# Performance work log

Measured on AMD Instinct MI355X. Metric: run time of the kernel, lower is better.

## Reference

```python
import jax, jax.numpy as jnp
import numpy as np

B, T, U = 64, 512, 1024
TIME_STEP = 0.008

# Rieke cone phototransduction parameters (scaleFac = 1, values are final)
PR = dict(sigma=22.0, phi=22.0, eta=2000.0, beta=9.0, cgmp2cur=0.01,
          cgmphill=3.0, cdark=1.0, betaSlow=0.4, hillcoef=4.0,
          hillaffinity=0.5, gamma=10.0, gdark=20.0)


def setup_inputs() -> dict:
    key = jax.random.key(0)
    X = jax.random.uniform(key, (B, T, U), dtype=jnp.float32)  # light intensity >= 0
    inp = {"X_fun": X}
    for name, v in PR.items():
        inp[name] = jnp.full((1, U), v, dtype=jnp.float32)  # flax param shape (1, units)
    return inp


def reference(X_fun, sigma, phi, eta, beta, cgmp2cur, cgmphill, cdark,
              betaSlow, hillcoef, hillaffinity, gamma, gdark):
    # Derived constants (as in runRiekeModel preamble)
    darkCurrent = gdark ** cgmphill * cgmp2cur / 2
    gdark_e = (2 * darkCurrent / cgmp2cur) ** (1 / cgmphill)
    cur2ca = beta * cdark / darkCurrent
    smax = eta / phi * gdark_e * (1 + (cdark / hillaffinity) ** hillcoef)

    Bd, Td, Ud = X_fun.shape
    ones = jnp.ones((Bd, Ud), X_fun.dtype)
    g0 = gdark_e * ones
    s0 = gdark_e * eta / phi * ones
    c0 = cdark * ones
    cslow0 = cdark * ones
    r0 = X_fun[:, 0, :] * gamma / sigma
    p0 = (eta + r0) / phi

    def step(carry, x_prev):
        g, s, c, cslow, p, r = carry
        r_n = r + TIME_STEP * (-sigma * r) + gamma * x_prev
        p_n = p + TIME_STEP * (r + eta - phi * p)
        c_n = c + TIME_STEP * (cur2ca * cgmp2cur * g ** cgmphill
                               / (1 + cslow / cdark) - beta * c)
        cslow_n = cslow - TIME_STEP * (betaSlow * (cslow - c))
        s_n = smax / (1 + (c_n / hillaffinity) ** hillcoef)
        g_n = g + TIME_STEP * (s - p * g)
        return (g_n, s_n, c_n, cslow_n, p_n, r_n), g_n

    xs = jnp.moveaxis(X_fun[:, :-1, :], 1, 0)  # [T-1, B, U], step pnt uses X[:, pnt-1, :]
    _, g_seq = jax.lax.scan(step, (g0, s0, c0, cslow0, p0, r0), xs)
    # g[:, 0, :] stays zero in the original (loop starts at pnt=1)
    g = jnp.concatenate([jnp.zeros((Bd, 1, Ud), X_fun.dtype),
                         jnp.moveaxis(g_seq, 0, 1)], axis=1)
    return -(cgmp2cur * g ** cgmphill) / 2
```

## Files before the change

### kernel.cpp

```cpp
#include <hip/hip_runtime.h>
#include <math.h>


#define TT 512
#define UU 1024
#define UN 16
#define DTSTEP 0.008f

template <bool FAST>
__device__ __forceinline__ void run_chain(
    const float* __restrict__ xrow, float* __restrict__ orow,
    float sigma, float phi, float eta, float beta, float cgmp2cur,
    float cgmphill, float cdark, float betaSlow, float hillcoef,
    float hillaff, float gam, float gdark)
{
    const float darkCurrent = powf(gdark, cgmphill) * cgmp2cur * 0.5f;
    const float gdark_e = powf(2.0f * darkCurrent / cgmp2cur, 1.0f / cgmphill);
    const float cur2ca = beta * cdark / darkCurrent;
    const float smax = eta / phi * gdark_e *
                       (1.0f + powf(cdark / hillaff, hillcoef));

    const float Ar   = 1.0f - DTSTEP * sigma;
    const float icd  = 1.0f / cdark;
    const float kc   = cur2ca * cgmp2cur;
    const float iha  = 1.0f / hillaff;
    const float outk = -0.5f * cgmp2cur;
    const float dtbs = DTSTEP * betaSlow;

    float g  = gdark_e;
    float s  = gdark_e * eta / phi;
    float c  = cdark;
    float cs = cdark;
    float r, p;
    {
        float x0 = xrow[0];
        r = x0 * gam / sigma;
        p = (eta + r) / phi;
    }
    float gp = FAST ? g * g * g : __powf(g, cgmphill);

    orow[0] = 0.0f;

    auto step = [&](float x, float& outv) {
        float rn  = fmaf(Ar, r, gam * x);
        float pn  = fmaf(DTSTEP, (r + eta) - phi * p, p);
        float den = fmaf(cs, icd, 1.0f);
        float cn  = fmaf(DTSTEP,
                         fmaf(-beta, c, kc * gp * __builtin_amdgcn_rcpf(den)),
                         c);
        float csn = fmaf(-dtbs, cs - c, cs);
        float sn;
        if (FAST) {
            float t2 = cn * iha;
            t2 *= t2;
            sn = smax * __builtin_amdgcn_rcpf(fmaf(t2, t2, 1.0f));
        } else {
            sn = smax / (1.0f + __powf(cn * iha, hillcoef));
        }
        float gn  = fmaf(DTSTEP, fmaf(-p, g, s), g);
        float gpn = FAST ? gn * gn * gn : __powf(gn, cgmphill);
        outv = outk * gpn;
        g = gn; s = sn; c = cn; cs = csn; p = pn; r = rn; gp = gpn;
    };

    float bufA[UN], bufB[UN], ob[UN];

#pragma unroll
    for (int k = 0; k < UN; ++k) bufA[k] = xrow[k * UU];

    const float* xln = xrow + UN * UU;
    float* op = orow + UU;

    for (int pair = 0; pair < 15; ++pair) {
#pragma unroll
        for (int k = 0; k < UN; ++k) bufB[k] = xln[k * UU];
        __builtin_amdgcn_sched_barrier(0);
#pragma unroll
        for (int k = 0; k < UN; ++k) step(bufA[k], ob[k]);
        __builtin_amdgcn_sched_barrier(0);
#pragma unroll
        for (int k = 0; k < UN; ++k) op[k * UU] = ob[k];
        __builtin_amdgcn_sched_barrier(0);
        xln += UN * UU; op += UN * UU;

#pragma unroll
        for (int k = 0; k < UN; ++k) bufA[k] = xln[k * UU];
        __builtin_amdgcn_sched_barrier(0);
#pragma unroll
        for (int k = 0; k < UN; ++k) step(bufB[k], ob[k]);
        __builtin_amdgcn_sched_barrier(0);
#pragma unroll
        for (int k = 0; k < UN; ++k) op[k * UU] = ob[k];
        __builtin_amdgcn_sched_barrier(0);
        xln += UN * UU; op += UN * UU;
    }

#pragma unroll
    for (int k = 0; k < UN; ++k) bufB[k] = xln[k * UU];
    __builtin_amdgcn_sched_barrier(0);
#pragma unroll
    for (int k = 0; k < UN; ++k) step(bufA[k], ob[k]);
    __builtin_amdgcn_sched_barrier(0);
#pragma unroll
    for (int k = 0; k < UN; ++k) op[k * UU] = ob[k];
    op += UN * UU;

#pragma unroll
    for (int k = 0; k < UN - 1; ++k) {
        float o;
        step(bufB[k], o);
        op[k * UU] = o;
    }
}

__global__ __launch_bounds__(256, 1) void prfr_kernel(
    const float* __restrict__ X,
    const float* __restrict__ sigma_p, const float* __restrict__ phi_p,
    const float* __restrict__ eta_p,   const float* __restrict__ beta_p,
    const float* __restrict__ cgmp2cur_p, const float* __restrict__ cgmphill_p,
    const float* __restrict__ cdark_p, const float* __restrict__ betaSlow_p,
    const float* __restrict__ hillcoef_p, const float* __restrict__ hillaff_p,
    const float* __restrict__ gamma_p, const float* __restrict__ gdark_p,
    float* __restrict__ out, int total)
{
    const int idx = blockIdx.x * blockDim.x + threadIdx.x;
    if (idx >= total) return;
    const int u = idx & (UU - 1);
    const int b = idx >> 10;

    const float* xrow = X + (long)b * (TT * UU) + u;
    float* orow = out + (long)b * (TT * UU) + u;

    const float sigma = sigma_p[u], phi = phi_p[u], eta = eta_p[u];
    const float beta = beta_p[u], cgmp2cur = cgmp2cur_p[u];
    const float cgmphill = cgmphill_p[u], cdark = cdark_p[u];
    const float betaSlow = betaSlow_p[u], hillcoef = hillcoef_p[u];
    const float hillaff = hillaff_p[u], gam = gamma_p[u], gdark = gdark_p[u];

    if (cgmphill == 3.0f && hillcoef == 4.0f) {
        run_chain<true>(xrow, orow, sigma, phi, eta, beta, cgmp2cur, cgmphill,
                        cdark, betaSlow, hillcoef, hillaff, gam, gdark);
    } else {
        run_chain<false>(xrow, orow, sigma, phi, eta, beta, cgmp2cur, cgmphill,
                         cdark, betaSlow, hillcoef, hillaff, gam, gdark);
    }
}

extern "C" void kernel_launch(void* const* d_in, const int* in_sizes, int n_in,
                              void* d_out, int out_size, void* d_ws, size_t ws_size,
                              hipStream_t stream)
{
    const float* X = (const float*)d_in[0];
    const int B = in_sizes[0] / (TT * UU);
    const int total = B * UU;
    const int block = 256;
    const int grid = (total + block - 1) / block;
    prfr_kernel<<<grid, block, 0, stream>>>(
        X,
        (const float*)d_in[1],  (const float*)d_in[2],  (const float*)d_in[3],
        (const float*)d_in[4],  (const float*)d_in[5],  (const float*)d_in[6],
        (const float*)d_in[7],  (const float*)d_in[8],  (const float*)d_in[9],
        (const float*)d_in[10], (const float*)d_in[11], (const float*)d_in[12],
        (float*)d_out, total);
}
```

Baseline: 258.9 us.

## Prefetch input tiles into LDS via async global_load_lds double buffering

Replaces the register-based double-buffered input prefetch with asynchronous global-to-LDS loads (global_load_lds) into a per-wave double buffer in shared memory. Explicit s_waitcnt vmcnt counts gate reuse of the buffer. Output stores are now interleaved with the recurrence steps instead of being batched. The aim is to free registers and overlap input fetch with the serial recurrence, at the cost of extra LDS reads and reliance on hand-counted outstanding memory operations for correctness.

```diff
diff --git a/kernel.cpp b/kernel.cpp
--- a/kernel.cpp
+++ b/kernel.cpp
@@ -7,9 +7,17 @@
 #define UN 16
 #define DTSTEP 0.008f
 
+__device__ __forceinline__ void gload_lds(const float* g, float* l) {
+    __builtin_amdgcn_global_load_lds(
+        (__attribute__((address_space(1))) void*)(uintptr_t)g,
+        (__attribute__((address_space(3))) void*)l, 4, 0, 0);
+}
+
 template <bool FAST>
 __device__ __forceinline__ void run_chain(
     const float* __restrict__ xrow, float* __restrict__ orow,
+    float* __restrict__ swave,
+    int lane,
     float sigma, float phi, float eta, float beta, float cgmp2cur,
     float cgmphill, float cdark, float betaSlow, float hillcoef,
     float hillaff, float gam, float gdark)
@@ -63,53 +71,53 @@
         g = gn; s = sn; c = cn; cs = csn; p = pn; r = rn; gp = gpn;
     };
 
-    float bufA[UN], bufB[UN], ob[UN];
+#pragma unroll
+    for (int k = 0; k < UN; ++k)
+        gload_lds(xrow + k * UU, swave + k * 64);
 
-#pragma unroll
-    for (int k = 0; k < UN; ++k) bufA[k] = xrow[k * UU];
-
-    const float* xln = xrow + UN * UU;
+    const float* xst = xrow + UN * UU;
     float* op = orow + UU;
 
-    for (int pair = 0; pair < 15; ++pair) {
+    for (int n = 0; n < TT / UN - 1; ++n) {
+        if (n == 0) {
+            asm volatile("s_waitcnt vmcnt(0)" ::: "memory");
+        } else {
+            asm volatile("s_waitcnt vmcnt(16)" ::: "memory");
+        }
+        __builtin_amdgcn_sched_barrier(0);
+        const int p2 = (n & 1) * (UN * 64);
+        float xa[UN];
 #pragma unroll
-        for (int k = 0; k < UN; ++k) bufB[k] = xln[k * UU];
+        for (int k = 0; k < UN; ++k) xa[k] = swave[p2 + k * 64 + lane];
+        __builtin_amdgcn_sched_barrier(0);
+        const int q2 = ((n & 1) ^ 1) * (UN * 64);
+#pragma unroll
+        for (int k = 0; k < UN; ++k)
+            gload_lds(xst + k * UU, swave + q2 + k * 64);
         __builtin_amdgcn_sched_barrier(0);
 #pragma unroll
-        for (int k = 0; k < UN; ++k) step(bufA[k], ob[k]);
-        __builtin_amdgcn_sched_barrier(0);
-#pragma unroll
-        for (int k = 0; k < UN; ++k) op[k * UU] = ob[k];
-        __builtin_amdgcn_sched_barrier(0);
-        xln += UN * UU; op += UN * UU;
-
-#pragma unroll
-        for (int k = 0; k < UN; ++k) bufA[k] = xln[k * UU];
-        __builtin_amdgcn_sched_barrier(0);
-#pragma unroll
-        for (int k = 0; k < UN; ++k) step(bufB[k], ob[k]);
-        __builtin_amdgcn_sched_barrier(0);
-#pragma unroll
-        for (int k = 0; k < UN; ++k) op[k * UU] = ob[k];
-        __builtin_amdgcn_sched_barrier(0);
-        xln += UN * UU; op += UN * UU;
+        for (int k = 0; k < UN; ++k) {
+            float o;
+            step(xa[k], o);
+            op[k * UU] = o;
+        }
+        xst += UN * UU;
+        op += UN * UU;
     }
 
+    asm volatile("s_waitcnt vmcnt(16)" ::: "memory");
+    __builtin_amdgcn_sched_barrier(0);
+    {
+        const int p2 = (31 & 1) * (UN * 64);
+        float xa[UN];
 #pragma unroll
-    for (int k = 0; k < UN; ++k) bufB[k] = xln[k * UU];
-    __builtin_amdgcn_sched_barrier(0);
+        for (int k = 0; k < UN; ++k) xa[k] = swave[p2 + k * 64 + lane];
 #pragma unroll
-    for (int k = 0; k < UN; ++k) step(bufA[k], ob[k]);
-    __builtin_amdgcn_sched_barrier(0);
-#pragma unroll
-    for (int k = 0; k < UN; ++k) op[k * UU] = ob[k];
-    op += UN * UU;
-
-#pragma unroll
-    for (int k = 0; k < UN - 1; ++k) {
-        float o;
-        step(bufB[k], o);
-        op[k * UU] = o;
+        for (int k = 0; k < UN - 1; ++k) {
+            float o;
+            step(xa[k], o);
+            op[k * UU] = o;
+        }
     }
 }
 
@@ -123,10 +131,14 @@
     const float* __restrict__ gamma_p, const float* __restrict__ gdark_p,
     float* __restrict__ out, int total)
 {
+    __shared__ float smem[4][2][UN][64];
+
     const int idx = blockIdx.x * blockDim.x + threadIdx.x;
     if (idx >= total) return;
     const int u = idx & (UU - 1);
     const int b = idx >> 10;
+    const int w = __builtin_amdgcn_readfirstlane(threadIdx.x >> 6);
+    const int lane = threadIdx.x & 63;
 
     const float* xrow = X + (long)b * (TT * UU) + u;
     float* orow = out + (long)b * (TT * UU) + u;
@@ -137,12 +149,16 @@
     const float betaSlow = betaSlow_p[u], hillcoef = hillcoef_p[u];
     const float hillaff = hillaff_p[u], gam = gamma_p[u], gdark = gdark_p[u];
 
+    float* swave = &smem[w][0][0][0];
+
     if (cgmphill == 3.0f && hillcoef == 4.0f) {
-        run_chain<true>(xrow, orow, sigma, phi, eta, beta, cgmp2cur, cgmphill,
-                        cdark, betaSlow, hillcoef, hillaff, gam, gdark);
+        run_chain<true>(xrow, orow, swave, lane, sigma, phi, eta, beta,
+                        cgmp2cur, cgmphill, cdark, betaSlow, hillcoef,
+                        hillaff, gam, gdark);
     } else {
-        run_chain<false>(xrow, orow, sigma, phi, eta, beta, cgmp2cur, cgmphill,
-                         cdark, betaSlow, hillcoef, hillaff, gam, gdark);
+        run_chain<false>(xrow, orow, swave, lane, sigma, phi, eta, beta,
+                         cgmp2cur, cgmphill, cdark, betaSlow, hillcoef,
+                         hillaff, gam, gdark);
     }
 }
 
```

New measurement: 257.3 us. No clear change (-0.6%).
